# Performance work log

Hardware: AMD Instinct MI355X
Metric: run time of the kernel (lower is better)

The kernel has to match this reference:

```python
import jax, jax.numpy as jnp
import numpy as np

N, E, G, D, L, T = 50000, 100000, 2000, 300, 5, 10
NUM_ATOM, NUM_CHIR, NUM_BOND, NUM_DIR = 120, 3, 6, 3


def setup_inputs() -> dict:
    key = jax.random.key(0)
    ks = jax.random.split(key, 24)
    s = 1.0 / np.sqrt(D)
    inp = {
        'x': jnp.stack([jax.random.randint(ks[0], (N,), 0, NUM_ATOM),
                        jax.random.randint(ks[1], (N,), 0, NUM_CHIR)], axis=1),
        'edge_index': jax.random.randint(ks[2], (2, E), 0, N),
        'edge_attr': jnp.stack([jax.random.randint(ks[3], (E,), 0, 4),
                                jax.random.randint(ks[4], (E,), 0, NUM_DIR)], axis=1),
        'batch': jnp.sort(jax.random.randint(ks[5], (N,), 0, G)),
        'x1': jnp.stack([jax.random.randint(ks[6], (N,), 0, NUM_ATOM),
                         jax.random.randint(ks[7], (N,), 0, NUM_CHIR)], axis=1),
        'edge_index1': jax.random.randint(ks[8], (2, E), 0, N),
        'edge_attr1': jnp.stack([jax.random.randint(ks[9], (E,), 0, 4),
                                 jax.random.randint(ks[10], (E,), 0, NUM_DIR)], axis=1),
        'batch1': jnp.sort(jax.random.randint(ks[11], (N,), 0, G)),
        'xemb1': jax.random.normal(ks[12], (NUM_ATOM, D)) * s,
        'xemb2': jax.random.normal(ks[13], (NUM_CHIR, D)) * s,
        'eemb1': jax.random.normal(ks[14], (L, NUM_BOND, D)) * s,
        'eemb2': jax.random.normal(ks[15], (L, NUM_DIR, D)) * s,
        'W1': jax.random.normal(ks[16], (L, D, 2 * D)) * s,
        'b1': jnp.zeros((L, 2 * D)),
        'W2': jax.random.normal(ks[17], (L, 2 * D, D)) * (1.0 / np.sqrt(2 * D)),
        'b2': jnp.zeros((L, D)),
        'gamma': jnp.ones((L, D)),
        'beta': jnp.zeros((L, D)),
        'predW': jax.random.normal(ks[18], (D, T)) * s,
        'predb': jnp.zeros((T,)),
    }
    return inp


def _gnn(xi, ei, ea, xemb1, xemb2, eemb1, eemb2, W1, b1, W2, b2, gamma, beta):
    n = xi.shape[0]
    h = xemb1[xi[:, 0]] + xemb2[xi[:, 1]]  # [N, D]
    loop = jnp.arange(n)
    src = jnp.concatenate([ei[0], loop])
    dst = jnp.concatenate([ei[1], loop])
    # self-loop edge attr = [4, 0]
    sl = jnp.concatenate([jnp.full((n, 1), 4, ea.dtype), jnp.zeros((n, 1), ea.dtype)], axis=1)
    eaf = jnp.concatenate([ea, sl], axis=0)
    for l in range(L):
        eemb = eemb1[l][eaf[:, 0]] + eemb2[l][eaf[:, 1]]     # [E+N, D]
        msg = h[src] + eemb                                   # gather
        agg = jax.ops.segment_sum(msg, dst, num_segments=n)   # scatter-add
        h2 = jax.nn.relu(agg @ W1[l] + b1[l]) @ W2[l] + b2[l] # GIN MLP
        mu = h2.mean(axis=0)
        var = ((h2 - mu) ** 2).mean(axis=0)                   # batchnorm (train stats)
        h2 = gamma[l] * (h2 - mu) * jax.lax.rsqrt(var + 1e-5) + beta[l]
        if l < L - 1:
            h2 = jax.nn.relu(h2)
        h = h2
    return h  # JK='last'


def _mean_pool(node_rep, batch):
    s = jax.ops.segment_sum(node_rep, batch, num_segments=G)
    cnt = jax.ops.segment_sum(jnp.ones((node_rep.shape[0],), node_rep.dtype), batch, num_segments=G)
    return s / jnp.maximum(cnt, 1.0)[:, None]


def reference(x, edge_index, edge_attr, batch, x1, edge_index1, edge_attr1, batch1,
              xemb1, xemb2, eemb1, eemb2, W1, b1, W2, b2, gamma, beta, predW, predb):
    node_rep = _gnn(x, edge_index, edge_attr, xemb1, xemb2, eemb1, eemb2, W1, b1, W2, b2, gamma, beta)
    node_rep1 = _gnn(x1, edge_index1, edge_attr1, xemb1, xemb2, eemb1, eemb2, W1, b1, W2, b2, gamma, beta)
    graph_rep = _mean_pool(node_rep, batch)
    graph_rep1 = _mean_pool(node_rep1, batch1)
    pred = graph_rep @ predW + predb
    pred1 = graph_rep1 @ predW + predb
    return (pred, graph_rep, node_rep, pred1, graph_rep1, node_rep1)
```

## Files before the change

kernel.cpp:

```cpp
#include <hip/hip_runtime.h>
#include <hip/hip_bf16.h>

typedef unsigned short ushort_t;
typedef short v8s __attribute__((ext_vector_type(8)));
typedef unsigned short v8u __attribute__((ext_vector_type(8)));
typedef unsigned short v4u __attribute__((ext_vector_type(4)));
typedef float v4f __attribute__((ext_vector_type(4)));

#define N_NODES 50000
#define N_EDGES 100000
#define N_GRAPH 2000
#define DIM     300
#define DIM2    600
#define NLAYER  5
#define NTASK   10
#define D4      75
#define D4P     80

#define LDA  304
#define LDY  608
#define LDAH 320
#define NPAD 50048

#define KB1 40
#define NT1 5
#define KB2 76
#define NT2 3
#define MT_TILES 391

#define AS1 __attribute__((address_space(1)))
#define AS3 __attribute__((address_space(3)))
static __device__ __forceinline__ void gload_lds16(const void* g, void* l) {
    __builtin_amdgcn_global_load_lds((AS1 void*)(g), (AS3 void*)(l), 16, 0, 0);
}

static __device__ __forceinline__ ushort_t f2bf(float f) {
    unsigned int u;
    __builtin_memcpy(&u, &f, 4);
    unsigned int lsb = (u >> 16) & 1u;
    u += 0x7fffu + lsb;
    return (ushort_t)(u >> 16);
}
static __device__ __forceinline__ void split2(float f, ushort_t& h, ushort_t& l) {
    unsigned int u;
    __builtin_memcpy(&u, &f, 4);
    h = (ushort_t)(u >> 16);
    unsigned int um = u & 0xFFFF0000u;
    float hf;
    __builtin_memcpy(&hf, &um, 4);
    float lf = f - hf;
    unsigned int ul;
    __builtin_memcpy(&ul, &lf, 4);
    l = (ushort_t)(ul >> 16);
}

static __device__ __forceinline__ int swz_wgid(int orig, int nwg) {
    int xcd = orig & 7;
    int seq = orig >> 3;
    int q = nwg >> 3, r = nwg & 7;
    int base = (xcd < r) ? xcd * (q + 1) : r * (q + 1) + (xcd - r) * q;
    return base + seq;
}

__global__ void k_embed_init(const int* __restrict__ x,
                             const float* __restrict__ xe1,
                             const float* __restrict__ xe2,
                             float* __restrict__ h) {
    int tid = blockIdx.x * blockDim.x + threadIdx.x;
    if (tid >= N_NODES * D4) return;
    int node = tid / D4;
    int d0 = (tid % D4) * 4;
    int i0 = x[node * 2 + 0];
    int i1 = x[node * 2 + 1];
    float4 a = *(const float4*)(xe1 + (size_t)i0 * DIM + d0);
    float4 b = *(const float4*)(xe2 + (size_t)i1 * DIM + d0);
    float4 o;
    o.x = a.x + b.x; o.y = a.y + b.y; o.z = a.z + b.z; o.w = a.w + b.w;
    *(float4*)(h + (size_t)node * LDA + d0) = o;
}

__global__ void k_deg(const int* __restrict__ ei, int* __restrict__ deg) {
    int e = blockIdx.x * blockDim.x + threadIdx.x;
    if (e >= N_EDGES) return;
    atomicAdd(&deg[ei[N_EDGES + e]], 1);
}

__global__ void k_scan1(const int* __restrict__ deg, int* __restrict__ excl,
                        int* __restrict__ blksum) {
    __shared__ int s[256];
    int i = blockIdx.x * 256 + threadIdx.x;
    int v = (i < N_NODES) ? deg[i] : 0;
    s[threadIdx.x] = v;
    __syncthreads();
#pragma unroll
    for (int o = 1; o < 256; o <<= 1) {
        int t = (threadIdx.x >= o) ? s[threadIdx.x - o] : 0;
        __syncthreads();
        s[threadIdx.x] += t;
        __syncthreads();
    }
    if (i < N_NODES) excl[i] = s[threadIdx.x] - v;
    if (threadIdx.x == 255) blksum[blockIdx.x] = s[255];
}

__global__ void k_scan2(int* __restrict__ blksum, int* __restrict__ blkoff, int nblk) {
    __shared__ int s[256];
    int v = (threadIdx.x < nblk) ? blksum[threadIdx.x] : 0;
    s[threadIdx.x] = v;
    __syncthreads();
#pragma unroll
    for (int o = 1; o < 256; o <<= 1) {
        int t = (threadIdx.x >= o) ? s[threadIdx.x - o] : 0;
        __syncthreads();
        s[threadIdx.x] += t;
        __syncthreads();
    }
    if (threadIdx.x < nblk) blkoff[threadIdx.x] = s[threadIdx.x] - v;
}

__global__ void k_scan3(const int* __restrict__ excl, const int* __restrict__ blkoff,
                        int* __restrict__ rowptr, int* __restrict__ fillptr) {
    int i = blockIdx.x * blockDim.x + threadIdx.x;
    if (i > N_NODES) return;
    int v = (i < N_NODES) ? (excl[i] + blkoff[i >> 8]) : N_EDGES;
    rowptr[i] = v;
    if (i < N_NODES) fillptr[i] = v;
}

__global__ void k_fill(const int* __restrict__ ei, const int* __restrict__ ea,
                       int* __restrict__ fillptr,
                       int* __restrict__ csrc, int* __restrict__ cea) {
    int e = blockIdx.x * blockDim.x + threadIdx.x;
    if (e >= N_EDGES) return;
    int dst = ei[N_EDGES + e];
    int pos = atomicAdd(&fillptr[dst], 1);
    csrc[pos] = ei[e];
    cea[pos] = (ea[2 * e + 0] << 16) | ea[2 * e + 1];
}

__global__ void k_gather_agg(const int* __restrict__ rowptr,
                             const int* __restrict__ csrc,
                             const int* __restrict__ cea,
                             const float* __restrict__ h,
                             const float* __restrict__ ee1,
                             const float* __restrict__ ee2,
                             const float* __restrict__ ee1sl,
                             const float* __restrict__ ee2sl,
                             ushort_t* __restrict__ aghi,
                             ushort_t* __restrict__ aglo) {
    int tid = blockIdx.x * blockDim.x + threadIdx.x;
    if (tid >= N_NODES * D4P) return;
    int node = tid / D4P;
    int c = tid % D4P;
    if (c >= D4) {
        v4u z = (v4u){0, 0, 0, 0};
        *(v4u*)(aghi + (size_t)node * LDAH + c * 4) = z;
        *(v4u*)(aglo + (size_t)node * LDAH + c * 4) = z;
        return;
    }
    int d0 = c * 4;
    float4 a = *(const float4*)(h + (size_t)node * LDA + d0);
    float4 e1 = *(const float4*)(ee1sl + d0);
    float4 e2 = *(const float4*)(ee2sl + d0);
    a.x += e1.x + e2.x; a.y += e1.y + e2.y; a.z += e1.z + e2.z; a.w += e1.w + e2.w;
    int p0 = rowptr[node], p1 = rowptr[node + 1];
    for (int p = p0; p < p1; ++p) {
        int src = csrc[p];
        int pk = cea[p];
        int a0 = pk >> 16, a1 = pk & 0xFFFF;
        float4 hv = *(const float4*)(h + (size_t)src * LDA + d0);
        float4 f1 = *(const float4*)(ee1 + (size_t)a0 * DIM + d0);
        float4 f2 = *(const float4*)(ee2 + (size_t)a1 * DIM + d0);
        a.x += hv.x + f1.x + f2.x;
        a.y += hv.y + f1.y + f2.y;
        a.z += hv.z + f1.z + f2.z;
        a.w += hv.w + f1.w + f2.w;
    }
    float av[4] = {a.x, a.y, a.z, a.w};
    v4u hh, ll;
#pragma unroll
    for (int i = 0; i < 4; ++i) {
        ushort_t uh, ul;
        split2(av[i], uh, ul);
        hh[i] = uh;
        ll[i] = ul;
    }
    *(v4u*)(aghi + (size_t)node * LDAH + d0) = hh;
    *(v4u*)(aglo + (size_t)node * LDAH + d0) = ll;
}

__global__ void k_pack_w(const float* __restrict__ W,
                         ushort_t* __restrict__ hi,
                         ushort_t* __restrict__ lo,
                         int K, int N, int KBv, int NTv, int total) {
    int idx = blockIdx.x * blockDim.x + threadIdx.x;
    if (idx >= total) return;
    int j = idx & 7;
    int n = (idx >> 3) & 127;
    int tmp = idx >> 10;
    int kb = tmp % KBv; tmp /= KBv;
    int nt = tmp % NTv;
    int l = tmp / NTv;
    int k = kb * 8 + j;
    int ng = nt * 128 + n;
    float v = 0.f;
    if (k < K && ng < N) v = W[((size_t)l * K + k) * N + ng];
    ushort_t h, lw;
    split2(v, h, lw);
    hi[idx] = h;
    lo[idx] = lw;
}

template <bool RELU, bool SPLITA, bool BNSTAT, typename OT>
__global__ __launch_bounds__(256) void k_gemm_mfma(
        const ushort_t* __restrict__ Ahi,
        const ushort_t* __restrict__ Alo,
        const ushort_t* __restrict__ Bhi,
        const ushort_t* __restrict__ Blo,
        const float* __restrict__ bias,
        OT* __restrict__ C,
        double* __restrict__ bnsum,
        double* __restrict__ bnsq,
        int M, int N, int Ksteps, int KBv, int NTv, int nwg,
        int lda, int ldc, int ncap) {
    alignas(16) __shared__ ushort_t sAhi[8192];
    alignas(16) __shared__ ushort_t sAlo[SPLITA ? 8192 : 16];
    alignas(16) __shared__ ushort_t sBhi[8192];
    alignas(16) __shared__ ushort_t sBlo[8192];

    const int wgid = swz_wgid(blockIdx.x, nwg);
    const int nt = wgid % NTv;
    const int mt = wgid / NTv;
    const int t = threadIdx.x;

    const int w = t >> 6;
    const int lane = t & 63;
    const int wm = w >> 1;
    const int wn = w & 1;
    const int quad = lane >> 4;
    const int lr = lane & 15;

    v4f acc[4][4];
#pragma unroll
    for (int i = 0; i < 4; ++i)
#pragma unroll
        for (int j = 0; j < 4; ++j) acc[i][j] = (v4f){0.f, 0.f, 0.f, 0.f};

    auto stage = [&](int buf, int ks) {
        const int kk = ks * 32;
        const int bo = buf * 4096;
        const size_t base = ((size_t)nt * KBv + ks * 4) * 1024;
#pragma unroll
        for (int p = 0; p < 2; ++p) {
            int o = p * 2048 + t * 8;
            gload_lds16(Bhi + base + o, &sBhi[bo + o]);
            gload_lds16(Blo + base + o, &sBlo[bo + o]);
        }
#pragma unroll
        for (int p = 0; p < 2; ++p) {
            int cidx = p * 256 + t;
            int kb = cidx >> 7;
            int m = cidx & 127;
            size_t go = (size_t)(mt * 128 + m) * lda + kk + kb * 8;
            gload_lds16(Ahi + go, &sAhi[bo + cidx * 8]);
            if (SPLITA) gload_lds16(Alo + go, &sAlo[bo + cidx * 8]);
        }
    };

    stage(0, 0);
    __syncthreads();
    int cur = 0;
    for (int ks = 0; ks < Ksteps; ++ks) {
        if (ks + 1 < Ksteps) stage(cur ^ 1, ks + 1);
        const int bo = cur * 4096;
        v8s a_hi[4], a_lo[4], b_hi[4], b_lo[4];
#pragma unroll
        for (int s = 0; s < 4; ++s) {
            a_hi[s] = *(const v8s*)&sAhi[bo + quad * 1024 + (wm * 64 + s * 16 + lr) * 8];
            if (SPLITA)
                a_lo[s] = *(const v8s*)&sAlo[bo + quad * 1024 + (wm * 64 + s * 16 + lr) * 8];
            b_hi[s] = *(const v8s*)&sBhi[bo + quad * 1024 + (wn * 64 + s * 16 + lr) * 8];
            b_lo[s] = *(const v8s*)&sBlo[bo + quad * 1024 + (wn * 64 + s * 16 + lr) * 8];
        }
#pragma unroll
        for (int si = 0; si < 4; ++si) {
#pragma unroll
            for (int sj = 0; sj < 4; ++sj) {
                acc[si][sj] = __builtin_amdgcn_mfma_f32_16x16x32_bf16(
                    a_hi[si], b_hi[sj], acc[si][sj], 0, 0, 0);
                acc[si][sj] = __builtin_amdgcn_mfma_f32_16x16x32_bf16(
                    a_hi[si], b_lo[sj], acc[si][sj], 0, 0, 0);
                if (SPLITA)
                    acc[si][sj] = __builtin_amdgcn_mfma_f32_16x16x32_bf16(
                        a_lo[si], b_hi[sj], acc[si][sj], 0, 0, 0);
            }
        }
        __syncthreads();
        cur ^= 1;
    }

    float bsum[4], bsq[4];
    if (BNSTAT) {
#pragma unroll
        for (int sj = 0; sj < 4; ++sj) { bsum[sj] = 0.f; bsq[sj] = 0.f; }
    }
#pragma unroll
    for (int sj = 0; sj < 4; ++sj) {
        int col = nt * 128 + wn * 64 + sj * 16 + lr;
        if (col >= ncap) continue;
        float bv = (col < N) ? bias[col] : 0.f;
#pragma unroll
        for (int si = 0; si < 4; ++si) {
#pragma unroll
            for (int r = 0; r < 4; ++r) {
                size_t row = (size_t)mt * 128 + wm * 64 + si * 16 + quad * 4 + r;
                float v = acc[si][sj][r] + bv;
                if (RELU) v = fmaxf(v, 0.f);
                if (BNSTAT && row < (size_t)M) { bsum[sj] += v; bsq[sj] += v * v; }
                if (sizeof(OT) == 2)
                    ((ushort_t*)C)[row * ldc + col] = f2bf(v);
                else
                    ((float*)C)[row * ldc + col] = v;
            }
        }
    }
    if (BNSTAT) {
        float* sred = (float*)sBhi;
#pragma unroll
        for (int sj = 0; sj < 4; ++sj) {
            bsum[sj] += __shfl_xor(bsum[sj], 16);
            bsum[sj] += __shfl_xor(bsum[sj], 32);
            bsq[sj]  += __shfl_xor(bsq[sj], 16);
            bsq[sj]  += __shfl_xor(bsq[sj], 32);
        }
        if (quad == 0) {
#pragma unroll
            for (int sj = 0; sj < 4; ++sj) {
                int idx = wm * 128 + wn * 64 + sj * 16 + lr;
                sred[idx] = bsum[sj];
                sred[256 + idx] = bsq[sj];
            }
        }
        __syncthreads();
        if (t < 128) {
            float s = sred[t] + sred[128 + t];
            float q = sred[256 + t] + sred[256 + 128 + t];
            int col = nt * 128 + t;
            if (col < N) {
                atomicAdd(&bnsum[col], (double)s);
                atomicAdd(&bnsq[col], (double)q);
            }
        }
    }
}

__global__ void k_bn_finalize(const double* __restrict__ sum,
                              const double* __restrict__ sumsq,
                              float* __restrict__ mean,
                              float* __restrict__ rstd) {
    int d = threadIdx.x;
    if (d >= DIM) return;
    double mu = sum[d] / (double)N_NODES;
    double var = sumsq[d] / (double)N_NODES - mu * mu;
    if (var < 0.0) var = 0.0;
    mean[d] = (float)mu;
    rstd[d] = (float)(1.0 / sqrt(var + 1e-5));
}

template <bool RELU, bool WOUT>
__global__ void k_bn_apply(const float* __restrict__ h2,
                           const float* __restrict__ mean,
                           const float* __restrict__ rstd,
                           const float* __restrict__ gamma,
                           const float* __restrict__ beta,
                           float* __restrict__ h,
                           float* __restrict__ nodeout) {
    int tid = blockIdx.x * blockDim.x + threadIdx.x;
    if (tid >= N_NODES * D4) return;
    int node = tid / D4;
    int d0 = (tid % D4) * 4;
    float4 v = *(const float4*)(h2 + (size_t)node * LDA + d0);
    float o[4] = {v.x, v.y, v.z, v.w};
    float4 r;
    float* rp = &r.x;
#pragma unroll
    for (int i = 0; i < 4; ++i) {
        int d = d0 + i;
        float u = (o[i] - mean[d]) * rstd[d] * gamma[d] + beta[d];
        if (RELU) u = fmaxf(u, 0.f);
        rp[i] = u;
    }
    *(float4*)(h + (size_t)node * LDA + d0) = r;
    if (WOUT) *(float4*)(nodeout + (size_t)node * DIM + d0) = r;
}

__global__ __launch_bounds__(256) void k_pool_seg(const float* __restrict__ h,
                                                  const int* __restrict__ batch,
                                                  float* __restrict__ pool,
                                                  float* __restrict__ gout) {
    __shared__ float4 s[3][D4];
    const int g = blockIdx.x;
    int lo = 0, hi = N_NODES;
    while (lo < hi) {
        int m = (lo + hi) >> 1;
        if (batch[m] < g) lo = m + 1; else hi = m;
    }
    const int p0 = lo;
    hi = N_NODES;
    while (lo < hi) {
        int m = (lo + hi) >> 1;
        if (batch[m] < g + 1) lo = m + 1; else hi = m;
    }
    const int p1 = lo;

    const int t = threadIdx.x;
    if (t < 3 * D4) {
        const int c = t % D4;
        const int rc = t / D4;
        const int d0 = c * 4;
        float4 acc = {0.f, 0.f, 0.f, 0.f};
        for (int r = p0 + rc; r < p1; r += 3) {
            float4 v = *(const float4*)(h + (size_t)r * LDA + d0);
            acc.x += v.x; acc.y += v.y; acc.z += v.z; acc.w += v.w;
        }
        s[rc][c] = acc;
    }
    __syncthreads();
    if (t < D4) {
        float4 a = s[0][t], b = s[1][t], c = s[2][t];
        const float inv = 1.0f / fmaxf((float)(p1 - p0), 1.0f);
        float4 r;
        r.x = (a.x + b.x + c.x) * inv;
        r.y = (a.y + b.y + c.y) * inv;
        r.z = (a.z + b.z + c.z) * inv;
        r.w = (a.w + b.w + c.w) * inv;
        *(float4*)(pool + (size_t)g * DIM + t * 4) = r;
        *(float4*)(gout + (size_t)g * DIM + t * 4) = r;
    }
}

__global__ void k_pred(const float* __restrict__ pool,
                       const float* __restrict__ predW,
                       const float* __restrict__ predb,
                       float* __restrict__ out) {
    int tid = blockIdx.x * blockDim.x + threadIdx.x;
    if (tid >= N_GRAPH * NTASK) return;
    int g = tid / NTASK;
    int tt = tid % NTASK;
    float s = predb[tt];
    const float* pr = pool + (size_t)g * DIM;
    for (int k = 0; k < DIM; ++k) s += pr[k] * predW[k * NTASK + tt];
    out[(size_t)g * NTASK + tt] = s;
}

static inline int cdiv(long long a, long long b) { return (int)((a + b - 1) / b); }

extern "C" void kernel_launch(void* const* d_in, const int* in_sizes, int n_in,
                              void* d_out, int out_size, void* d_ws, size_t ws_size,
                              hipStream_t stream) {
    const int* x    = (const int*)d_in[0];
    const int* ei   = (const int*)d_in[1];
    const int* ea   = (const int*)d_in[2];
    const int* bat  = (const int*)d_in[3];
    const int* x1   = (const int*)d_in[4];
    const int* ei1  = (const int*)d_in[5];
    const int* ea1  = (const int*)d_in[6];
    const int* bat1 = (const int*)d_in[7];
    const float* xemb1 = (const float*)d_in[8];
    const float* xemb2 = (const float*)d_in[9];
    const float* eemb1 = (const float*)d_in[10];
    const float* eemb2 = (const float*)d_in[11];
    const float* W1    = (const float*)d_in[12];
    const float* b1    = (const float*)d_in[13];
    const float* W2    = (const float*)d_in[14];
    const float* b2    = (const float*)d_in[15];
    const float* gamma = (const float*)d_in[16];
    const float* beta  = (const float*)d_in[17];
    const float* predW = (const float*)d_in[18];
    const float* predb = (const float*)d_in[19];
    float* out = (float*)d_out;

    char* ws = (char*)d_ws;
    size_t off = 0;
    auto take = [&](size_t bytes) -> char* {
        char* p = ws + off;
        off += (bytes + 255) & ~(size_t)255;
        return p;
    };
    float* h      = (float*)take((size_t)NPAD * LDA * 4);
    ushort_t* aghi = (ushort_t*)take((size_t)NPAD * LDAH * 2 * 2);
    ushort_t* aglo = aghi + (size_t)NPAD * LDAH;
    ushort_t* y   = (ushort_t*)h;
    float* h2     = (float*)aghi;
    float* pool   = (float*)take((size_t)N_GRAPH * DIM * 4);
    double* bnsum = (double*)take(DIM * 8 * 2);
    double* bnsq  = bnsum + DIM;
    float* bnmean = (float*)take(DIM * 4 * 2);
    float* bnrstd = bnmean + DIM;
    const size_t W1P = (size_t)NLAYER * NT1 * KB1 * 1024;
    const size_t W2P = (size_t)NLAYER * NT2 * KB2 * 1024;
    ushort_t* w1hi = (ushort_t*)take(W1P * 2);
    ushort_t* w1lo = (ushort_t*)take(W1P * 2);
    ushort_t* w2hi = (ushort_t*)take(W2P * 2);
    ushort_t* w2lo = (ushort_t*)take(W2P * 2);
    int* deg     = (int*)take(N_NODES * 4);
    int* excl    = (int*)take(N_NODES * 4);
    int* blksum  = (int*)take(256 * 4);
    int* blkoff  = (int*)take(256 * 4);
    int* fillptr = (int*)take(N_NODES * 4);
    int* rowptr0 = (int*)take((N_NODES + 1) * 4);
    int* csrc0   = (int*)take(N_EDGES * 4);
    int* cea0    = (int*)take(N_EDGES * 4);
    int* rowptr1 = (int*)take((N_NODES + 1) * 4);
    int* csrc1   = (int*)take(N_EDGES * 4);
    int* cea1    = (int*)take(N_EDGES * 4);
    (void)ws_size; (void)in_sizes; (void)n_in; (void)out_size;

    const int TB = 256;
    const int gN75 = cdiv((long long)N_NODES * D4, TB);
    const int gN80 = cdiv((long long)N_NODES * D4P, TB);
    const int gE   = cdiv(N_EDGES, TB);
    const int gScan = cdiv(N_NODES, TB);
    const int gScan3 = cdiv(N_NODES + 1, TB);
    const int NWG1 = NT1 * MT_TILES;
    const int NWG2 = NT2 * MT_TILES;

    k_pack_w<<<cdiv((long long)W1P, TB), TB, 0, stream>>>(W1, w1hi, w1lo, DIM, DIM2, KB1, NT1, (int)W1P);
    k_pack_w<<<cdiv((long long)W2P, TB), TB, 0, stream>>>(W2, w2hi, w2lo, DIM2, DIM, KB2, NT2, (int)W2P);

    auto build_csr = [&](const int* eip, const int* eap, int* rowptr, int* csrc, int* cea) {
        hipMemsetAsync(deg, 0, N_NODES * 4, stream);
        k_deg<<<gE, TB, 0, stream>>>(eip, deg);
        k_scan1<<<gScan, TB, 0, stream>>>(deg, excl, blksum);
        k_scan2<<<1, 256, 0, stream>>>(blksum, blkoff, gScan);
        k_scan3<<<gScan3, TB, 0, stream>>>(excl, blkoff, rowptr, fillptr);
        k_fill<<<gE, TB, 0, stream>>>(eip, eap, fillptr, csrc, cea);
    };
    build_csr(ei, ea, rowptr0, csrc0, cea0);
    build_csr(ei1, ea1, rowptr1, csrc1, cea1);

    auto run_gnn = [&](const int* xp, const int* batp,
                       const int* rowptr, const int* csrc, const int* cea,
                       float* out_pred, float* out_graph, float* out_node) {
        k_embed_init<<<gN75, TB, 0, stream>>>(xp, xemb1, xemb2, h);
        for (int l = 0; l < NLAYER; ++l) {
            const float* ee1l = eemb1 + (size_t)l * 6 * DIM;
            const float* ee2l = eemb2 + (size_t)l * 3 * DIM;
            k_gather_agg<<<gN80, TB, 0, stream>>>(rowptr, csrc, cea, h,
                                                  ee1l, ee2l, ee1l + 4 * DIM, ee2l,
                                                  aghi, aglo);
            k_gemm_mfma<true, true, false, ushort_t>
                <<<NWG1, TB, 0, stream>>>(
                    aghi, aglo,
                    w1hi + (size_t)l * NT1 * KB1 * 1024, w1lo + (size_t)l * NT1 * KB1 * 1024,
                    b1 + (size_t)l * DIM2, y, nullptr, nullptr,
                    N_NODES, DIM2, 10, KB1, NT1, NWG1, LDAH, LDY, LDY);
            hipMemsetAsync(bnsum, 0, DIM * 8 * 2, stream);
            k_gemm_mfma<false, false, true, float>
                <<<NWG2, TB, 0, stream>>>(
                    y, y,
                    w2hi + (size_t)l * NT2 * KB2 * 1024, w2lo + (size_t)l * NT2 * KB2 * 1024,
                    b2 + (size_t)l * DIM, h2, bnsum, bnsq,
                    N_NODES, DIM, 19, KB2, NT2, NWG2, LDY, LDA, LDA);
            k_bn_finalize<<<1, 512, 0, stream>>>(bnsum, bnsq, bnmean, bnrstd);
            if (l < NLAYER - 1)
                k_bn_apply<true, false><<<gN75, TB, 0, stream>>>(
                    h2, bnmean, bnrstd, gamma + (size_t)l * DIM, beta + (size_t)l * DIM, h, nullptr);
            else
                k_bn_apply<false, true><<<gN75, TB, 0, stream>>>(
                    h2, bnmean, bnrstd, gamma + (size_t)l * DIM, beta + (size_t)l * DIM, h, out_node);
        }
        k_pool_seg<<<N_GRAPH, TB, 0, stream>>>(h, batp, pool, out_graph);
        k_pred<<<cdiv((long long)N_GRAPH * NTASK, TB), TB, 0, stream>>>(pool, predW, predb, out_pred);
    };

    const size_t GT = (size_t)N_GRAPH * NTASK;
    const size_t GD = (size_t)N_GRAPH * DIM;
    const size_t ND = (size_t)N_NODES * DIM;
    run_gnn(x, bat, rowptr0, csrc0, cea0, out, out + GT, out + GT + GD);
    run_gnn(x1, bat1, rowptr1, csrc1, cea1,
            out + GT + GD + ND, out + 2 * GT + GD + ND, out + 2 * GT + 2 * GD + ND);
}
```

Measured before the change: 2.175 ms.

## Fuse batchnorm apply into gather and pooling; read lo operands from global

Removes the separate batchnorm-apply kernel. Normalisation and ReLU are now applied on the fly inside the next layer's gather-aggregate, and the final layer's normalisation is folded into the pooling kernel, which also writes the node output. Two ping-pong buffers replace the fixed h/h2 aliasing. The GEMM no longer stages the low-precision A/B halves in LDS. It loads them directly from global memory into registers, halving LDS use, and asks for 4 blocks per CU via launch bounds. The gather now recomputes batchnorm for every neighbour it reads, and the uncached global loads of the lo halves may add latency to the MFMA loop.

After: 4.182 ms. 1.92x slower.

```diff
diff --git a/kernel.cpp b/kernel.cpp
--- a/kernel.cpp
+++ b/kernel.cpp
@@ -138,14 +138,19 @@
     cea[pos] = (ea[2 * e + 0] << 16) | ea[2 * e + 1];
 }
 
+template <bool BN>
 __global__ void k_gather_agg(const int* __restrict__ rowptr,
                              const int* __restrict__ csrc,
                              const int* __restrict__ cea,
-                             const float* __restrict__ h,
+                             const float* __restrict__ hin,
                              const float* __restrict__ ee1,
                              const float* __restrict__ ee2,
                              const float* __restrict__ ee1sl,
                              const float* __restrict__ ee2sl,
+                             const float* __restrict__ bnmean,
+                             const float* __restrict__ bnrstd,
+                             const float* __restrict__ bngam,
+                             const float* __restrict__ bnbet,
                              ushort_t* __restrict__ aghi,
                              ushort_t* __restrict__ aglo) {
     int tid = blockIdx.x * blockDim.x + threadIdx.x;
@@ -159,7 +164,23 @@
         return;
     }
     int d0 = c * 4;
-    float4 a = *(const float4*)(h + (size_t)node * LDA + d0);
+    float4 m4, r4, g4, b4;
+    if (BN) {
+        m4 = *(const float4*)(bnmean + d0);
+        r4 = *(const float4*)(bnrstd + d0);
+        g4 = *(const float4*)(bngam + d0);
+        b4 = *(const float4*)(bnbet + d0);
+    }
+    auto bn4 = [&](float4 v) -> float4 {
+        if (BN) {
+            v.x = fmaxf((v.x - m4.x) * r4.x * g4.x + b4.x, 0.f);
+            v.y = fmaxf((v.y - m4.y) * r4.y * g4.y + b4.y, 0.f);
+            v.z = fmaxf((v.z - m4.z) * r4.z * g4.z + b4.z, 0.f);
+            v.w = fmaxf((v.w - m4.w) * r4.w * g4.w + b4.w, 0.f);
+        }
+        return v;
+    };
+    float4 a = bn4(*(const float4*)(hin + (size_t)node * LDA + d0));
     float4 e1 = *(const float4*)(ee1sl + d0);
     float4 e2 = *(const float4*)(ee2sl + d0);
     a.x += e1.x + e2.x; a.y += e1.y + e2.y; a.z += e1.z + e2.z; a.w += e1.w + e2.w;
@@ -168,7 +189,7 @@
         int src = csrc[p];
         int pk = cea[p];
         int a0 = pk >> 16, a1 = pk & 0xFFFF;
-        float4 hv = *(const float4*)(h + (size_t)src * LDA + d0);
+        float4 hv = bn4(*(const float4*)(hin + (size_t)src * LDA + d0));
         float4 f1 = *(const float4*)(ee1 + (size_t)a0 * DIM + d0);
         float4 f2 = *(const float4*)(ee2 + (size_t)a1 * DIM + d0);
         a.x += hv.x + f1.x + f2.x;
@@ -212,7 +233,7 @@
 }
 
 template <bool RELU, bool SPLITA, bool BNSTAT, typename OT>
-__global__ __launch_bounds__(256) void k_gemm_mfma(
+__global__ __launch_bounds__(256, 4) void k_gemm_mfma(
         const ushort_t* __restrict__ Ahi,
         const ushort_t* __restrict__ Alo,
         const ushort_t* __restrict__ Bhi,
@@ -224,9 +245,7 @@
         int M, int N, int Ksteps, int KBv, int NTv, int nwg,
         int lda, int ldc, int ncap) {
     alignas(16) __shared__ ushort_t sAhi[8192];
-    alignas(16) __shared__ ushort_t sAlo[SPLITA ? 8192 : 16];
     alignas(16) __shared__ ushort_t sBhi[8192];
-    alignas(16) __shared__ ushort_t sBlo[8192];
 
     const int wgid = swz_wgid(blockIdx.x, nwg);
     const int nt = wgid % NTv;
@@ -254,7 +273,6 @@
         for (int p = 0; p < 2; ++p) {
             int o = p * 2048 + t * 8;
             gload_lds16(Bhi + base + o, &sBhi[bo + o]);
-            gload_lds16(Blo + base + o, &sBlo[bo + o]);
         }
 #pragma unroll
         for (int p = 0; p < 2; ++p) {
@@ -263,7 +281,6 @@
             int m = cidx & 127;
             size_t go = (size_t)(mt * 128 + m) * lda + kk + kb * 8;
             gload_lds16(Ahi + go, &sAhi[bo + cidx * 8]);
-            if (SPLITA) gload_lds16(Alo + go, &sAlo[bo + cidx * 8]);
         }
     };
 
@@ -271,29 +288,42 @@
     __syncthreads();
     int cur = 0;
     for (int ks = 0; ks < Ksteps; ++ks) {
-        if (ks + 1 < Ksteps) stage(cur ^ 1, ks + 1);
+        const int kk = ks * 32;
         const int bo = cur * 4096;
-        v8s a_hi[4], a_lo[4], b_hi[4], b_lo[4];
+        v8s a_hi[4], b_hi[4], a_lo[4], b_lo[4];
 #pragma unroll
         for (int s = 0; s < 4; ++s) {
             a_hi[s] = *(const v8s*)&sAhi[bo + quad * 1024 + (wm * 64 + s * 16 + lr) * 8];
+            b_hi[s] = *(const v8s*)&sBhi[bo + quad * 1024 + (wn * 64 + s * 16 + lr) * 8];
+        }
+#pragma unroll
+        for (int s = 0; s < 4; ++s) {
+            b_lo[s] = *(const v8s*)(Blo + ((size_t)(nt * KBv + ks * 4 + quad)) * 1024 +
+                                    (wn * 64 + s * 16 + lr) * 8);
             if (SPLITA)
-                a_lo[s] = *(const v8s*)&sAlo[bo + quad * 1024 + (wm * 64 + s * 16 + lr) * 8];
-            b_hi[s] = *(const v8s*)&sBhi[bo + quad * 1024 + (wn * 64 + s * 16 + lr) * 8];
-            b_lo[s] = *(const v8s*)&sBlo[bo + quad * 1024 + (wn * 64 + s * 16 + lr) * 8];
-        }
-#pragma unroll
-        for (int si = 0; si < 4; ++si) {
-#pragma unroll
-            for (int sj = 0; sj < 4; ++sj) {
+                a_lo[s] = *(const v8s*)(Alo + (size_t)(mt * 128 + wm * 64 + s * 16 + lr) * lda +
+                                        kk + quad * 8);
+        }
+        if (ks + 1 < Ksteps) stage(cur ^ 1, ks + 1);
+#pragma unroll
+        for (int si = 0; si < 4; ++si)
+#pragma unroll
+            for (int sj = 0; sj < 4; ++sj)
                 acc[si][sj] = __builtin_amdgcn_mfma_f32_16x16x32_bf16(
                     a_hi[si], b_hi[sj], acc[si][sj], 0, 0, 0);
+#pragma unroll
+        for (int si = 0; si < 4; ++si)
+#pragma unroll
+            for (int sj = 0; sj < 4; ++sj)
                 acc[si][sj] = __builtin_amdgcn_mfma_f32_16x16x32_bf16(
                     a_hi[si], b_lo[sj], acc[si][sj], 0, 0, 0);
-                if (SPLITA)
+        if (SPLITA) {
+#pragma unroll
+            for (int si = 0; si < 4; ++si)
+#pragma unroll
+                for (int sj = 0; sj < 4; ++sj)
                     acc[si][sj] = __builtin_amdgcn_mfma_f32_16x16x32_bf16(
                         a_lo[si], b_hi[sj], acc[si][sj], 0, 0, 0);
-            }
         }
         __syncthreads();
         cur ^= 1;
@@ -367,37 +397,15 @@
     rstd[d] = (float)(1.0 / sqrt(var + 1e-5));
 }
 
-template <bool RELU, bool WOUT>
-__global__ void k_bn_apply(const float* __restrict__ h2,
-                           const float* __restrict__ mean,
-                           const float* __restrict__ rstd,
-                           const float* __restrict__ gamma,
-                           const float* __restrict__ beta,
-                           float* __restrict__ h,
-                           float* __restrict__ nodeout) {
-    int tid = blockIdx.x * blockDim.x + threadIdx.x;
-    if (tid >= N_NODES * D4) return;
-    int node = tid / D4;
-    int d0 = (tid % D4) * 4;
-    float4 v = *(const float4*)(h2 + (size_t)node * LDA + d0);
-    float o[4] = {v.x, v.y, v.z, v.w};
-    float4 r;
-    float* rp = &r.x;
-#pragma unroll
-    for (int i = 0; i < 4; ++i) {
-        int d = d0 + i;
-        float u = (o[i] - mean[d]) * rstd[d] * gamma[d] + beta[d];
-        if (RELU) u = fmaxf(u, 0.f);
-        rp[i] = u;
-    }
-    *(float4*)(h + (size_t)node * LDA + d0) = r;
-    if (WOUT) *(float4*)(nodeout + (size_t)node * DIM + d0) = r;
-}
-
-__global__ __launch_bounds__(256) void k_pool_seg(const float* __restrict__ h,
-                                                  const int* __restrict__ batch,
-                                                  float* __restrict__ pool,
-                                                  float* __restrict__ gout) {
+__global__ __launch_bounds__(256) void k_bn_pool(const float* __restrict__ h2,
+                                                 const int* __restrict__ batch,
+                                                 const float* __restrict__ mean,
+                                                 const float* __restrict__ rstd,
+                                                 const float* __restrict__ gam,
+                                                 const float* __restrict__ bet,
+                                                 float* __restrict__ nodeout,
+                                                 float* __restrict__ pool,
+                                                 float* __restrict__ gout) {
     __shared__ float4 s[3][D4];
     const int g = blockIdx.x;
     int lo = 0, hi = N_NODES;
@@ -418,9 +426,18 @@
         const int c = t % D4;
         const int rc = t / D4;
         const int d0 = c * 4;
+        float4 m4 = *(const float4*)(mean + d0);
+        float4 r4 = *(const float4*)(rstd + d0);
+        float4 g4 = *(const float4*)(gam + d0);
+        float4 b4 = *(const float4*)(bet + d0);
         float4 acc = {0.f, 0.f, 0.f, 0.f};
         for (int r = p0 + rc; r < p1; r += 3) {
-            float4 v = *(const float4*)(h + (size_t)r * LDA + d0);
+            float4 v = *(const float4*)(h2 + (size_t)r * LDA + d0);
+            v.x = (v.x - m4.x) * r4.x * g4.x + b4.x;
+            v.y = (v.y - m4.y) * r4.y * g4.y + b4.y;
+            v.z = (v.z - m4.z) * r4.z * g4.z + b4.z;
+            v.w = (v.w - m4.w) * r4.w * g4.w + b4.w;
+            *(float4*)(nodeout + (size_t)r * DIM + d0) = v;
             acc.x += v.x; acc.y += v.y; acc.z += v.z; acc.w += v.w;
         }
         s[rc][c] = acc;
@@ -487,11 +504,9 @@
         off += (bytes + 255) & ~(size_t)255;
         return p;
     };
-    float* h      = (float*)take((size_t)NPAD * LDA * 4);
-    ushort_t* aghi = (ushort_t*)take((size_t)NPAD * LDAH * 2 * 2);
-    ushort_t* aglo = aghi + (size_t)NPAD * LDAH;
-    ushort_t* y   = (ushort_t*)h;
-    float* h2     = (float*)aghi;
+    const size_t BUFSZ = (size_t)NPAD * LDAH * 2 * 2;
+    char* bufA = take(BUFSZ);
+    char* bufB = take(BUFSZ);
     float* pool   = (float*)take((size_t)N_GRAPH * DIM * 4);
     double* bnsum = (double*)take(DIM * 8 * 2);
     double* bnsq  = bnsum + DIM;
@@ -542,35 +557,45 @@
     auto run_gnn = [&](const int* xp, const int* batp,
                        const int* rowptr, const int* csrc, const int* cea,
                        float* out_pred, float* out_graph, float* out_node) {
-        k_embed_init<<<gN75, TB, 0, stream>>>(xp, xemb1, xemb2, h);
+        k_embed_init<<<gN75, TB, 0, stream>>>(xp, xemb1, xemb2, (float*)bufA);
         for (int l = 0; l < NLAYER; ++l) {
+            char* pb = (l & 1) ? bufA : bufB;
+            char* yb = (l & 1) ? bufB : bufA;
+            ushort_t* aghi = (ushort_t*)pb;
+            ushort_t* aglo = aghi + (size_t)NPAD * LDAH;
+            const float* gin = (const float*)yb;
+            ushort_t* yv = (ushort_t*)yb;
+            float* h2v = (float*)pb;
             const float* ee1l = eemb1 + (size_t)l * 6 * DIM;
             const float* ee2l = eemb2 + (size_t)l * 3 * DIM;
-            k_gather_agg<<<gN80, TB, 0, stream>>>(rowptr, csrc, cea, h,
-                                                  ee1l, ee2l, ee1l + 4 * DIM, ee2l,
-                                                  aghi, aglo);
+            if (l == 0)
+                k_gather_agg<false><<<gN80, TB, 0, stream>>>(
+                    rowptr, csrc, cea, gin, ee1l, ee2l, ee1l + 4 * DIM, ee2l,
+                    nullptr, nullptr, nullptr, nullptr, aghi, aglo);
+            else
+                k_gather_agg<true><<<gN80, TB, 0, stream>>>(
+                    rowptr, csrc, cea, gin, ee1l, ee2l, ee1l + 4 * DIM, ee2l,
+                    bnmean, bnrstd, gamma + (size_t)(l - 1) * DIM, beta + (size_t)(l - 1) * DIM,
+                    aghi, aglo);
             k_gemm_mfma<true, true, false, ushort_t>
                 <<<NWG1, TB, 0, stream>>>(
                     aghi, aglo,
                     w1hi + (size_t)l * NT1 * KB1 * 1024, w1lo + (size_t)l * NT1 * KB1 * 1024,
-                    b1 + (size_t)l * DIM2, y, nullptr, nullptr,
+                    b1 + (size_t)l * DIM2, yv, nullptr, nullptr,
                     N_NODES, DIM2, 10, KB1, NT1, NWG1, LDAH, LDY, LDY);
             hipMemsetAsync(bnsum, 0, DIM * 8 * 2, stream);
             k_gemm_mfma<false, false, true, float>
                 <<<NWG2, TB, 0, stream>>>(
-                    y, y,
+                    yv, yv,
                     w2hi + (size_t)l * NT2 * KB2 * 1024, w2lo + (size_t)l * NT2 * KB2 * 1024,
-                    b2 + (size_t)l * DIM, h2, bnsum, bnsq,
+                    b2 + (size_t)l * DIM, h2v, bnsum, bnsq,
                     N_NODES, DIM, 19, KB2, NT2, NWG2, LDY, LDA, LDA);
             k_bn_finalize<<<1, 512, 0, stream>>>(bnsum, bnsq, bnmean, bnrstd);
-            if (l < NLAYER - 1)
-                k_bn_apply<true, false><<<gN75, TB, 0, stream>>>(
-                    h2, bnmean, bnrstd, gamma + (size_t)l * DIM, beta + (size_t)l * DIM, h, nullptr);
-            else
-                k_bn_apply<false, true><<<gN75, TB, 0, stream>>>(
-                    h2, bnmean, bnrstd, gamma + (size_t)l * DIM, beta + (size_t)l * DIM, h, out_node);
-        }
-        k_pool_seg<<<N_GRAPH, TB, 0, stream>>>(h, batp, pool, out_graph);
+        }
+        k_bn_pool<<<N_GRAPH, TB, 0, stream>>>(
+            (const float*)bufB, batp, bnmean, bnrstd,
+            gamma + (size_t)(NLAYER - 1) * DIM, beta + (size_t)(NLAYER - 1) * DIM,
+            out_node, pool, out_graph);
         k_pred<<<cdiv((long long)N_GRAPH * NTASK, TB), TB, 0, stream>>>(pool, predW, predb, out_pred);
     };
 
```
